# Optimization experiments

Measured on AMD Instinct MI355X. Metric: run time of the kernel, lower is better.

Reference implementation:

```python
import jax, jax.numpy as jnp
import numpy as np

N, E, D_IN, D_H, D_OUT = 50000, 600000, 128, 128, 1


def setup_inputs() -> dict:
    key = jax.random.key(0)
    ks = jax.random.split(key, 12)
    s = 1.0 / np.sqrt(D_H)
    inp = {
        "x": jax.random.normal(ks[0], (N, D_IN), dtype=jnp.float32),
        "edge_index": jax.random.randint(ks[1], (2, E), 0, N, dtype=jnp.int64),
        # GCNConv layer weights (in->h, h->h, h->h)
        "W0": jax.random.normal(ks[2], (D_IN, D_H), dtype=jnp.float32) * s,
        "b0": jnp.zeros((D_H,), dtype=jnp.float32),
        "W1": jax.random.normal(ks[3], (D_H, D_H), dtype=jnp.float32) * s,
        "b1": jnp.zeros((D_H,), dtype=jnp.float32),
        "W2": jax.random.normal(ks[4], (D_H, D_H), dtype=jnp.float32) * s,
        "b2": jnp.zeros((D_H,), dtype=jnp.float32),
        # MLP head
        "mlp_w1": jax.random.normal(ks[5], (D_H, D_H), dtype=jnp.float32) * s,
        "mlp_b1": jnp.zeros((D_H,), dtype=jnp.float32),
        "mlp_w2": jax.random.normal(ks[6], (D_H, D_OUT), dtype=jnp.float32) * s,
        "mlp_b2": jnp.zeros((D_OUT,), dtype=jnp.float32),
    }
    return inp


def reference(x, edge_index, W0, b0, W1, b1, W2, b2, mlp_w1, mlp_b1, mlp_w2, mlp_b2):
    n = x.shape[0]
    loop = jnp.arange(n, dtype=edge_index.dtype)
    # add self-loops (PyG GCNConv default)
    src = jnp.concatenate([edge_index[0], loop])
    dst = jnp.concatenate([edge_index[1], loop])
    # symmetric normalization: deg counts incoming edges incl. self-loop
    deg = jax.ops.segment_sum(jnp.ones(src.shape, dtype=x.dtype), dst, num_segments=n)
    dinv = jax.lax.rsqrt(deg)  # deg >= 1 due to self-loops
    norm = (dinv[src] * dinv[dst])[:, None]  # [E+N, 1]

    def gcn_conv(h, W, b):
        h = h @ W                       # [N, d]
        msg = h[src] * norm             # gather + scale, [E+N, d]
        return jax.ops.segment_sum(msg, dst, num_segments=n) + b

    # num_layers=3: first two convs with ReLU (dropout is identity in eval)
    h = jax.nn.relu(gcn_conv(x, W0, b0))
    h = jax.nn.relu(gcn_conv(h, W1, b1))
    h = gcn_conv(h, W2, b2)
    # MLP head (dropout identity in eval)
    h = jax.nn.relu(h @ mlp_w1 + mlp_b1)
    return h @ mlp_w2 + mlp_b2
```

## Files before the change

### kernel.cpp

```cpp
#include <hip/hip_runtime.h>
#include <hip/hip_fp16.h>

constexpr int D = 128;

typedef _Float16 half8 __attribute__((ext_vector_type(8)));
typedef float f32x4 __attribute__((ext_vector_type(4)));


__global__ void k_zero(int4* __restrict__ p, int n4) {
    int i = blockIdx.x * 256 + threadIdx.x;
    if (i < n4) p[i] = make_int4(0, 0, 0, 0);
}


__global__ void k_count(const int* __restrict__ dst, int* __restrict__ cnt, int E) {
    int e = blockIdx.x * 256 + threadIdx.x;
    if (e < E) atomicAdd(&cnt[dst[e]], 1);
}

__global__ __launch_bounds__(256) void k_deg_stats(const int* __restrict__ cnt,
                                                   float* __restrict__ dinv,
                                                   int* __restrict__ bsum, int n) {
    __shared__ int sm[256];
    int tid = threadIdx.x;
    int i = blockIdx.x * 256 + tid;
    int c = (i < n) ? cnt[i] : 0;
    if (i < n) dinv[i] = rsqrtf((float)(c + 1));
    sm[tid] = c;
    __syncthreads();
    for (int off = 128; off > 0; off >>= 1) {
        if (tid < off) sm[tid] += sm[tid + off];
        __syncthreads();
    }
    if (tid == 0) bsum[blockIdx.x] = sm[0];
}

__global__ __launch_bounds__(256) void k_local_scan2(const int* __restrict__ cnt,
                                                     const int* __restrict__ bsum, int nb,
                                                     int* __restrict__ rowptr,
                                                     int* __restrict__ cursor, int n) {
    __shared__ int sb[256];
    __shared__ int sm[256];
    int tid = threadIdx.x;
    int bid = blockIdx.x;
    int bv = (tid < nb) ? bsum[tid] : 0;
    sb[tid] = bv;
    __syncthreads();
    for (int off = 1; off < 256; off <<= 1) {
        int t = (tid >= off) ? sb[tid - off] : 0;
        __syncthreads();
        sb[tid] += t;
        __syncthreads();
    }
    int blockoff = (bid > 0) ? sb[bid - 1] : 0;
    int i = bid * 256 + tid;
    int v = (i < n) ? cnt[i] : 0;
    sm[tid] = v;
    __syncthreads();
    for (int off = 1; off < 256; off <<= 1) {
        int t = (tid >= off) ? sm[tid - off] : 0;
        __syncthreads();
        sm[tid] += t;
        __syncthreads();
    }
    if (i < n) {
        int rp = blockoff + sm[tid] - v;
        rowptr[i] = rp;
        cursor[i] = rp;
    }
    if (bid == 0 && tid == 0) rowptr[n] = sb[nb - 1];
}


template <typename IdxT>
__global__ __launch_bounds__(256) void k_prep(
    const int* __restrict__ src, const int* __restrict__ dst, int* __restrict__ cursor,
    IdxT* __restrict__ csr, int E, const float* __restrict__ x,
    const float* __restrict__ dinv, __half* __restrict__ xh, int n4,
    const float* __restrict__ W0, const float* __restrict__ W1,
    const float* __restrict__ W2, const float* __restrict__ M1,
    const float* __restrict__ b2, const float* __restrict__ c1,
    __half* __restrict__ Wf0, __half* __restrict__ Wf1, __half* __restrict__ Wfp,
    float* __restrict__ cp) {
    int T = gridDim.x * 256;
    int gid = blockIdx.x * 256 + threadIdx.x;

    for (int e = gid; e < E; e += T) {
        int s = src[e], d = dst[e];
        int p = atomicAdd(&cursor[d], 1);
        csr[p] = (IdxT)s;
    }

    for (int i = gid; i < n4; i += T) {
        float4 v = reinterpret_cast<const float4*>(x)[i];
        float dd = dinv[i >> 5];
        __half ho[4] = {__float2half(v.x * dd), __float2half(v.y * dd),
                        __float2half(v.z * dd), __float2half(v.w * dd)};
        reinterpret_cast<uint2*>(xh)[i] = *reinterpret_cast<uint2*>(ho);
    }

    for (int q = gid; q < 2 * 16384; q += T) {
        int m = q >> 14;
        int idx = q & 16383;
        int j = idx & 7;
        int l = (idx >> 3) & 63;
        int c = (idx >> 9) & 7;
        int kk = (idx >> 12) & 3;
        int row = kk * 32 + (l >> 4) * 8 + j;
        int col = c * 16 + (l & 15);
        const float* W = (m == 0) ? W0 : W1;
        __half* Wf = (m == 0) ? Wf0 : Wf1;
        Wf[idx] = __float2half(W[row * 128 + col]);
    }

    for (int idx = gid; idx < 16384; idx += T) {
        int j = idx & 7;
        int l = (idx >> 3) & 63;
        int c = (idx >> 9) & 7;
        int kk = (idx >> 12) & 3;
        int row = kk * 32 + (l >> 4) * 8 + j;
        int col = c * 16 + (l & 15);
        float acc = 0.f;
        for (int k = 0; k < 128; ++k)
            acc = fmaf(W2[row * 128 + k], M1[k * 128 + col], acc);
        Wfp[idx] = __float2half(acc);
    }

    if (gid < 128) {
        float acc = c1[gid];
        for (int k = 0; k < 128; ++k) acc = fmaf(b2[k], M1[k * 128 + gid], acc);
        cp[gid] = acc;
    }
}


__device__ inline void accm(float* a, uint4 g, float m) {
    float2 p0 = __half22float2(*reinterpret_cast<const __half2*>(&g.x));
    float2 p1 = __half22float2(*reinterpret_cast<const __half2*>(&g.y));
    float2 p2 = __half22float2(*reinterpret_cast<const __half2*>(&g.z));
    float2 p3 = __half22float2(*reinterpret_cast<const __half2*>(&g.w));
    a[0] = fmaf(m, p0.x, a[0]);
    a[1] = fmaf(m, p0.y, a[1]);
    a[2] = fmaf(m, p1.x, a[2]);
    a[3] = fmaf(m, p1.y, a[3]);
    a[4] = fmaf(m, p2.x, a[4]);
    a[5] = fmaf(m, p2.y, a[5]);
    a[6] = fmaf(m, p3.x, a[6]);
    a[7] = fmaf(m, p3.y, a[7]);
}

template <typename IdxT>
__global__ __launch_bounds__(256) void k_agg_h4(const uint4* __restrict__ Ah4,
                                                const int* __restrict__ rowptr,
                                                const IdxT* __restrict__ csr,
                                                const float* __restrict__ dinv,
                                                uint4* __restrict__ outh4, int n) {
    int wv = threadIdx.x >> 6;
    int lane = threadIdx.x & 63;
    int i = blockIdx.x * 4 + wv;
    if (i >= n) return;
    int qg = lane >> 4;
    int fl = lane & 15;
    float a[8];
#pragma unroll
    for (int j = 0; j < 8; ++j) a[j] = 0.f;
    int beg = rowptr[i], end = rowptr[i + 1];
    for (int base = beg; base < end; base += 64) {
        int cnt = end - base;
        if (cnt > 64) cnt = 64;
        int idxv = (base + lane < end) ? (int)csr[base + lane] : 0;
        for (int e = 0; e < cnt; e += 16) {
            int k0 = e + qg;
            int k1 = e + qg + 4;
            int k2 = e + qg + 8;
            int k3 = e + qg + 12;
            int s0 = __shfl(idxv, k0);
            int s1 = __shfl(idxv, k1);
            int s2 = __shfl(idxv, k2);
            int s3 = __shfl(idxv, k3);
            uint4 g0 = Ah4[s0 * 16 + fl];
            uint4 g1 = Ah4[s1 * 16 + fl];
            uint4 g2 = Ah4[s2 * 16 + fl];
            uint4 g3 = Ah4[s3 * 16 + fl];
            float m0 = (k0 < cnt) ? 1.f : 0.f;
            float m1 = (k1 < cnt) ? 1.f : 0.f;
            float m2 = (k2 < cnt) ? 1.f : 0.f;
            float m3 = (k3 < cnt) ? 1.f : 0.f;
            accm(a, g0, m0);
            accm(a, g1, m1);
            accm(a, g2, m2);
            accm(a, g3, m3);
        }
    }
#pragma unroll
    for (int j = 0; j < 8; ++j) {
        a[j] += __shfl_xor(a[j], 16);
        a[j] += __shfl_xor(a[j], 32);
    }
    if (qg == 0) {
        uint4 gs = Ah4[i * 16 + fl];
        accm(a, gs, 1.f);
        float di = dinv[i];
        __half ho[8];
#pragma unroll
        for (int j = 0; j < 8; ++j) ho[j] = __float2half(di * a[j]);
        outh4[i * 16 + fl] = *reinterpret_cast<const uint4*>(ho);
    }
}


template <int MODE>
__global__ __launch_bounds__(256) void k_gemm_mfma(const __half* __restrict__ A,
                                                   const __half* __restrict__ Wf,
                                                   const float* __restrict__ bias,
                                                   const float* __restrict__ dinv,
                                                   const float* __restrict__ m2,
                                                   const float* __restrict__ m2b,
                                                   void* __restrict__ outv, int n) {
    int tid = threadIdx.x;
    int w = tid >> 6;
    int l = tid & 63;
    int r0 = blockIdx.x * 64 + w * 16;
    int arow = r0 + (l & 15);
    if (arow > n - 1) arow = n - 1;
    int kb = (l >> 4) * 8;

    f32x4 acc[8];
#pragma unroll
    for (int c = 0; c < 8; ++c) acc[c] = (f32x4){0.f, 0.f, 0.f, 0.f};

#pragma unroll
    for (int kk = 0; kk < 4; ++kk) {
        half8 a = *reinterpret_cast<const half8*>(&A[arow * 128 + kk * 32 + kb]);
#pragma unroll
        for (int c = 0; c < 8; ++c) {
            half8 b = *reinterpret_cast<const half8*>(&Wf[((kk * 8 + c) * 64 + l) * 8]);
            acc[c] = __builtin_amdgcn_mfma_f32_16x16x32_f16(a, b, acc[c], 0, 0, 0);
        }
    }

    float bv[8];
#pragma unroll
    for (int c = 0; c < 8; ++c) bv[c] = bias[c * 16 + (l & 15)];

    if (MODE == 0) {
        __half* outh = (__half*)outv;
#pragma unroll
        for (int reg = 0; reg < 4; ++reg) {
            int r = r0 + (l >> 4) * 4 + reg;
            if (r < n) {
                float dr = dinv[r];
#pragma unroll
                for (int c = 0; c < 8; ++c) {
                    float v = dr * fmaxf(acc[c][reg] + bv[c], 0.f);
                    outh[r * 128 + c * 16 + (l & 15)] = __float2half(v);
                }
            }
        }
    } else {
        float* out = (float*)outv;
        float mv[8];
#pragma unroll
        for (int c = 0; c < 8; ++c) mv[c] = m2[c * 16 + (l & 15)];
        float m2bv = m2b[0];
#pragma unroll
        for (int reg = 0; reg < 4; ++reg) {
            float p = 0.f;
#pragma unroll
            for (int c = 0; c < 8; ++c)
                p = fmaf(fmaxf(acc[c][reg] + bv[c], 0.f), mv[c], p);
            p += __shfl_xor(p, 1);
            p += __shfl_xor(p, 2);
            p += __shfl_xor(p, 4);
            p += __shfl_xor(p, 8);
            int r = r0 + (l >> 4) * 4 + reg;
            if ((l & 15) == 0 && r < n) out[r] = p + m2bv;
        }
    }
}


extern "C" void kernel_launch(void* const* d_in, const int* in_sizes, int n_in,
                              void* d_out, int out_size, void* d_ws, size_t ws_size,
                              hipStream_t stream) {
    const float* x = (const float*)d_in[0];
    const int* ei = (const int*)d_in[1];
    const float* W0 = (const float*)d_in[2];
    const float* b0 = (const float*)d_in[3];
    const float* W1 = (const float*)d_in[4];
    const float* b1 = (const float*)d_in[5];
    const float* W2 = (const float*)d_in[6];
    const float* b2 = (const float*)d_in[7];
    const float* M1 = (const float*)d_in[8];
    const float* c1 = (const float*)d_in[9];
    const float* m2 = (const float*)d_in[10];
    const float* m2b = (const float*)d_in[11];
    float* out = (float*)d_out;

    int N = in_sizes[0] / D;
    int E = in_sizes[1] / 2;
    const int* src = ei;
    const int* dst = ei + E;

    char* ws = (char*)d_ws;
    size_t off = 0;
    auto alloc = [&](size_t bytes) -> void* {
        void* p = ws + off;
        off += (bytes + 255) & ~(size_t)255;
        return p;
    };

    int gN = (N + 255) / 256;
    int gE = (E + 255) / 256;
    int gAgg = (N + 3) / 4;
    int gGemm = (N + 63) / 64;
    int nElem4 = N * D / 4;

    __half* xh = (__half*)alloc((size_t)N * D * 2);
    __half* tbuf = (__half*)alloc((size_t)N * D * 2);
    __half* gbuf = (__half*)alloc((size_t)N * D * 2);
    int* cnt = (int*)alloc((size_t)N * 4);
    float* dinv = (float*)alloc((size_t)N * 4);
    int* rowptr = (int*)alloc((size_t)(N + 1) * 4);
    int* cursor = (int*)alloc((size_t)N * 4);
    void* csr = alloc((size_t)E * 4);
    float* cp = (float*)alloc((size_t)D * 4);
    __half* Wf0 = (__half*)alloc((size_t)D * D * 2);
    __half* Wf1 = (__half*)alloc((size_t)D * D * 2);
    __half* Wfp = (__half*)alloc((size_t)D * D * 2);
    int* bsum = (int*)alloc((size_t)gN * 4);

    bool small_idx = (N <= 65535);

    int zc = (N + 3) / 4;
    k_zero<<<(zc + 255) / 256, 256, 0, stream>>>((int4*)cnt, zc);
    k_count<<<gE, 256, 0, stream>>>(dst, cnt, E);
    k_deg_stats<<<gN, 256, 0, stream>>>(cnt, dinv, bsum, N);
    k_local_scan2<<<gN, 256, 0, stream>>>(cnt, bsum, gN, rowptr, cursor, N);
    if (small_idx)
        k_prep<ushort><<<2048, 256, 0, stream>>>(src, dst, cursor, (ushort*)csr, E, x,
                                                 dinv, xh, nElem4, W0, W1, W2, M1, b2,
                                                 c1, Wf0, Wf1, Wfp, cp);
    else
        k_prep<uint><<<2048, 256, 0, stream>>>(src, dst, cursor, (uint*)csr, E, x, dinv,
                                               xh, nElem4, W0, W1, W2, M1, b2, c1, Wf0,
                                               Wf1, Wfp, cp);

    auto agg = [&](const __half* in_h, __half* out_t) {
        if (small_idx)
            k_agg_h4<ushort><<<gAgg, 256, 0, stream>>>((const uint4*)in_h, rowptr,
                                                       (const ushort*)csr, dinv,
                                                       (uint4*)out_t, N);
        else
            k_agg_h4<uint><<<gAgg, 256, 0, stream>>>((const uint4*)in_h, rowptr,
                                                     (const uint*)csr, dinv,
                                                     (uint4*)out_t, N);
    };

    agg(xh, tbuf);
    k_gemm_mfma<0><<<gGemm, 256, 0, stream>>>(tbuf, Wf0, b0, dinv, nullptr, nullptr,
                                              gbuf, N);
    agg(gbuf, tbuf);
    k_gemm_mfma<0><<<gGemm, 256, 0, stream>>>(tbuf, Wf1, b1, dinv, nullptr, nullptr,
                                              gbuf, N);
    agg(gbuf, tbuf);
    k_gemm_mfma<1><<<gGemm, 256, 0, stream>>>(tbuf, Wfp, cp, dinv, m2, m2b, out, N);
}
```

Before: 187.3 us.

## Partition degree count and CSR fill atomics by destination range per XCD

Degree counting and CSR fill now assign each of 8 block groups (blockIdx & 7, assumed to map to one XCD) a contiguous destination-node range. Every group scans all edges and performs atomics only for destinations in its range, so atomic targets stay in one XCD's L2 instead of bouncing across dies. CSR fill is split out of k_prep into its own kernel, and k_prep now handles only the x conversion and weight prep, with fewer blocks. In exchange, every edge's dst is read eight times and one more kernel launch is added.

```diff
diff --git a/kernel.cpp b/kernel.cpp
--- a/kernel.cpp
+++ b/kernel.cpp
@@ -13,9 +13,45 @@
 }
 
 
-__global__ void k_count(const int* __restrict__ dst, int* __restrict__ cnt, int E) {
-    int e = blockIdx.x * 256 + threadIdx.x;
-    if (e < E) atomicAdd(&cnt[dst[e]], 1);
+__global__ __launch_bounds__(256) void k_count_xcd(const int* __restrict__ dst,
+                                                   int* __restrict__ cnt, int E, int n) {
+    int xcd = blockIdx.x & 7;
+    int chunk = blockIdx.x >> 3;
+    int nchunk = gridDim.x >> 3;
+    int lo = (int)((long long)n * xcd >> 3);
+    int hi = (int)((long long)n * (xcd + 1) >> 3);
+    int per = (E + nchunk - 1) / nchunk;
+    int e0 = chunk * per;
+    int e1 = e0 + per;
+    if (e1 > E) e1 = E;
+    for (int e = e0 + threadIdx.x; e < e1; e += 256) {
+        int d = dst[e];
+        if (d >= lo && d < hi) atomicAdd(&cnt[d], 1);
+    }
+}
+
+template <typename IdxT>
+__global__ __launch_bounds__(256) void k_fill_xcd(const int* __restrict__ src,
+                                                  const int* __restrict__ dst,
+                                                  int* __restrict__ cursor,
+                                                  IdxT* __restrict__ csr, int E, int n) {
+    int xcd = blockIdx.x & 7;
+    int chunk = blockIdx.x >> 3;
+    int nchunk = gridDim.x >> 3;
+    int lo = (int)((long long)n * xcd >> 3);
+    int hi = (int)((long long)n * (xcd + 1) >> 3);
+    int per = (E + nchunk - 1) / nchunk;
+    int e0 = chunk * per;
+    int e1 = e0 + per;
+    if (e1 > E) e1 = E;
+    for (int e = e0 + threadIdx.x; e < e1; e += 256) {
+        int d = dst[e];
+        if (d >= lo && d < hi) {
+            int s = src[e];
+            int p = atomicAdd(&cursor[d], 1);
+            csr[p] = (IdxT)s;
+        }
+    }
 }
 
 __global__ __launch_bounds__(256) void k_deg_stats(const int* __restrict__ cnt,
@@ -72,24 +108,15 @@
 }
 
 
-template <typename IdxT>
 __global__ __launch_bounds__(256) void k_prep(
-    const int* __restrict__ src, const int* __restrict__ dst, int* __restrict__ cursor,
-    IdxT* __restrict__ csr, int E, const float* __restrict__ x,
-    const float* __restrict__ dinv, __half* __restrict__ xh, int n4,
-    const float* __restrict__ W0, const float* __restrict__ W1,
-    const float* __restrict__ W2, const float* __restrict__ M1,
-    const float* __restrict__ b2, const float* __restrict__ c1,
-    __half* __restrict__ Wf0, __half* __restrict__ Wf1, __half* __restrict__ Wfp,
-    float* __restrict__ cp) {
+    const float* __restrict__ x, const float* __restrict__ dinv,
+    __half* __restrict__ xh, int n4, const float* __restrict__ W0,
+    const float* __restrict__ W1, const float* __restrict__ W2,
+    const float* __restrict__ M1, const float* __restrict__ b2,
+    const float* __restrict__ c1, __half* __restrict__ Wf0, __half* __restrict__ Wf1,
+    __half* __restrict__ Wfp, float* __restrict__ cp) {
     int T = gridDim.x * 256;
     int gid = blockIdx.x * 256 + threadIdx.x;
-
-    for (int e = gid; e < E; e += T) {
-        int s = src[e], d = dst[e];
-        int p = atomicAdd(&cursor[d], 1);
-        csr[p] = (IdxT)s;
-    }
 
     for (int i = gid; i < n4; i += T) {
         float4 v = reinterpret_cast<const float4*>(x)[i];
@@ -311,7 +338,6 @@
     };
 
     int gN = (N + 255) / 256;
-    int gE = (E + 255) / 256;
     int gAgg = (N + 3) / 4;
     int gGemm = (N + 63) / 64;
     int nElem4 = N * D / 4;
@@ -334,17 +360,15 @@
 
     int zc = (N + 3) / 4;
     k_zero<<<(zc + 255) / 256, 256, 0, stream>>>((int4*)cnt, zc);
-    k_count<<<gE, 256, 0, stream>>>(dst, cnt, E);
+    k_count_xcd<<<1024, 256, 0, stream>>>(dst, cnt, E, N);
     k_deg_stats<<<gN, 256, 0, stream>>>(cnt, dinv, bsum, N);
     k_local_scan2<<<gN, 256, 0, stream>>>(cnt, bsum, gN, rowptr, cursor, N);
     if (small_idx)
-        k_prep<ushort><<<2048, 256, 0, stream>>>(src, dst, cursor, (ushort*)csr, E, x,
-                                                 dinv, xh, nElem4, W0, W1, W2, M1, b2,
-                                                 c1, Wf0, Wf1, Wfp, cp);
+        k_fill_xcd<ushort><<<1024, 256, 0, stream>>>(src, dst, cursor, (ushort*)csr, E, N);
     else
-        k_prep<uint><<<2048, 256, 0, stream>>>(src, dst, cursor, (uint*)csr, E, x, dinv,
-                                               xh, nElem4, W0, W1, W2, M1, b2, c1, Wf0,
-                                               Wf1, Wfp, cp);
+        k_fill_xcd<uint><<<1024, 256, 0, stream>>>(src, dst, cursor, (uint*)csr, E, N);
+    k_prep<<<1024, 256, 0, stream>>>(x, dinv, xh, nElem4, W0, W1, W2, M1, b2, c1, Wf0,
+                                     Wf1, Wfp, cp);
 
     auto agg = [&](const __half* in_h, __half* out_t) {
         if (small_idx)
```

After: 196.2 us. 4.7% more time.
